# Optimization experiments

Measured on AMD Instinct MI355X. Metric: run time of the kernel, lower is better.

The kernel has to match this reference:

```python
import jax, jax.numpy as jnp
import numpy as np

B, C, E, HLR, WLR = 2, 64, 4, 192, 192


def setup_inputs() -> dict:
    key = jax.random.key(0)
    ks = jax.random.split(key, 8)
    s = 0.05  # keep activations/offsets in a sane range
    return {
        "x": jax.random.normal(ks[0], (B, C, HLR, WLR), jnp.float32),
        "fused": jax.random.normal(ks[1], (B, C, HLR, WLR), jnp.float32),
        "weight_compress": jax.random.normal(ks[2], (E, C // 8, C), jnp.float32) * s,
        "weight_expand": jax.random.normal(ks[3], (E, C, C // 8), jnp.float32) * s,
        "body_w1": jax.random.normal(ks[4], (64, 4), jnp.float32) * s,
        "body_b1": jnp.zeros((64,), jnp.float32),
        "body_w2": jax.random.normal(ks[5], (64, 64), jnp.float32) * s,
        "body_b2": jnp.zeros((64,), jnp.float32),
        "routing_w": jax.random.normal(ks[6], (E, 64), jnp.float32) * s,
        "routing_b": jnp.zeros((E,), jnp.float32),
        "offset_w": jax.random.normal(ks[7], (2, 64), jnp.float32) * s,
        "offset_b": jnp.zeros((2,), jnp.float32),
        "scale": 2,
    }


def _conv1x1(x, w, b):
    # x: [n, cin, H, W], w: [cout, cin] (1x1 conv)
    return jnp.einsum('oc,nchw->nohw', w, x) + b[None, :, None, None]


def _grid_sample(img, px, py):
    # Bilinear sample, align_corners=True semantics, zeros padding.
    # img: [b,c,h,w]; px, py: [b,H,W] absolute LR pixel coords.
    b, c, h, w = img.shape
    x0 = jnp.floor(px)
    y0 = jnp.floor(py)
    wx = (px - x0)[:, None]  # [b,1,H,W]
    wy = (py - y0)[:, None]

    def gather(xi, yi):
        valid = (xi >= 0) & (xi <= w - 1) & (yi >= 0) & (yi <= h - 1)
        xc = jnp.clip(xi, 0, w - 1).astype(jnp.int32)
        yc = jnp.clip(yi, 0, h - 1).astype(jnp.int32)
        v = jax.vmap(lambda im, yy, xx: im[:, yy, xx])(img, yc, xc)  # [b,c,H,W]
        return v * valid[:, None].astype(img.dtype)

    v00 = gather(x0, y0)
    v01 = gather(x0 + 1, y0)
    v10 = gather(x0, y0 + 1)
    v11 = gather(x0 + 1, y0 + 1)
    top = v00 * (1 - wx) + v01 * wx
    bot = v10 * (1 - wx) + v11 * wx
    return top * (1 - wy) + bot * wy


def reference(x, fused, weight_compress, weight_expand, body_w1, body_b1,
              body_w2, body_b2, routing_w, routing_b, offset_w, offset_b, scale):
    b, c, h, w = fused.shape
    H, W = round(h * scale), round(w * scale)
    e, c8 = weight_compress.shape[0], weight_compress.shape[1]

    ch = jnp.arange(H, dtype=jnp.float32)
    cw = jnp.arange(W, dtype=jnp.float32)
    coor_h = (ch + 0.5) / scale - jnp.floor((ch + 0.5) / scale + 0.001) - 0.5  # [H]
    coor_w = (cw + 0.5) / scale - jnp.floor((cw + 0.5) / scale + 0.001) - 0.5  # [W]
    inp = jnp.stack([
        jnp.full((H, W), 1.0 / scale, jnp.float32),
        jnp.full((H, W), 1.0 / scale, jnp.float32),
        jnp.broadcast_to(coor_h[:, None], (H, W)),
        jnp.broadcast_to(coor_w[None, :], (H, W)),
    ], 0)[None]  # [1,4,H,W]

    emb = jax.nn.relu(_conv1x1(inp, body_w1, body_b1))
    emb = jax.nn.relu(_conv1x1(emb, body_w2, body_b2))
    offset = _conv1x1(emb, offset_w, offset_b)            # [1,2,H,W]
    routing = jax.nn.sigmoid(_conv1x1(emb, routing_w, routing_b))  # [1,E,H,W]

    rw = routing.reshape(e, H * W).T                      # [HW, E]
    wc = (rw @ weight_compress.reshape(e, -1)).reshape(H, W, c8, c)  # per-pixel compress
    we = (rw @ weight_expand.reshape(e, -1)).reshape(H, W, c, c8)    # per-pixel expand

    # deformable sample: HR grid projected into LR space + learned offset (pixel units)
    px = jnp.broadcast_to((cw[None, :] + 0.5) / scale - 0.5, (H, W))[None] + offset[:, 0]
    py = jnp.broadcast_to((ch[:, None] + 0.5) / scale - 0.5, (H, W))[None] + offset[:, 1]
    px = jnp.broadcast_to(px, (b, H, W))
    py = jnp.broadcast_to(py, (b, H, W))
    fea0 = _grid_sample(fused, px, py)                    # [b,c,H,W]

    fea = fea0.transpose(0, 2, 3, 1)                      # [b,H,W,c]
    mid = jnp.einsum('hwoc,bhwc->bhwo', wc, fea)          # [b,H,W,c//8]
    out = jnp.einsum('hwco,bhwo->bhwc', we, mid)          # [b,H,W,c]
    return out.transpose(0, 3, 1, 2) + fea0
```

## Files before the change

### kernel.cpp

```cpp
#include <hip/hip_runtime.h>
#include <hip/hip_fp16.h>
#include <math.h>

typedef __attribute__((ext_vector_type(8))) _Float16 half8;
typedef __attribute__((ext_vector_type(4))) float f32x4;

#define HLR_ 192
#define WLR_ 192
#define H_ 384
#define W_ 384
#define LRP (HLR_*WLR_)
#define TPX 96
#define NTW (W_/TPX)
#define IPW 48
#define NCOL 52

#define WS_OFF_OFF 8192

__device__ __forceinline__ unsigned short f32_f16(float x){
    union { _Float16 h; unsigned short u; } c; c.h = (_Float16)x; return c.u;
}
__device__ __forceinline__ unsigned int pk_f16(float a, float b){
    union { _Float16 h[2]; unsigned int u; } c;
    c.h[0] = (_Float16)a; c.h[1] = (_Float16)b; return c.u;
}
__device__ __forceinline__ half8 splat8h(_Float16 h){
    half8 v = {h,h,h,h,h,h,h,h};
    return v;
}

__global__ __launch_bounds__(256) void prep_kernel(
    const float* __restrict__ w1, const float* __restrict__ b1,
    const float* __restrict__ w2, const float* __restrict__ b2,
    const float* __restrict__ rw, const float* __restrict__ rb,
    const float* __restrict__ ow, const float* __restrict__ ob,
    const float* __restrict__ WC, const float* __restrict__ WE,
    unsigned short* __restrict__ Kmat, float* __restrict__ g_off)
{
    __shared__ float smem[8912];
    int tid = threadIdx.x;

    float* sW2 = smem;
    float* sRW = smem + 4160;
    float* sE1 = smem + 4544;
    float* sR  = smem + 4800;
    float* sWc = smem + 4816;
    float* sWe = smem + 6864;

    for (int idx = tid; idx < 4096; idx += 256)
        sW2[(idx>>6)*65 + (idx&63)] = w2[idx];
    sRW[tid] = rw[tid];
    if (tid < 128) sRW[256 + tid] = ow[tid];

    int wave = tid >> 6, lane = tid & 63;
    int ph = wave >> 1, pw = wave & 1;

    float ch = (ph + 0.5f)*0.5f;
    float coor_h = ch - floorf(ch + 0.001f) - 0.5f;
    float cw = (pw + 0.5f)*0.5f;
    float coor_w = cw - floorf(cw + 0.001f) - 0.5f;

    float e1 = w1[lane*4+0]*0.5f + w1[lane*4+1]*0.5f
             + w1[lane*4+2]*coor_h + w1[lane*4+3]*coor_w + b1[lane];
    sE1[wave*64 + lane] = fmaxf(e1, 0.0f);
    __syncthreads();

    float e2 = b2[lane];
    #pragma unroll 16
    for (int i = 0; i < 64; ++i) e2 += sW2[lane*65 + i] * sE1[wave*64 + i];
    e2 = fmaxf(e2, 0.0f);

    #pragma unroll
    for (int k = 0; k < 6; ++k) {
        float t = sRW[k*64 + lane] * e2;
        #pragma unroll
        for (int m = 1; m <= 32; m <<= 1) t += __shfl_xor(t, m, 64);
        if (lane == 0) {
            if (k < 4) sR[wave*4 + k] = 1.0f/(1.0f + expf(-(t + rb[k])));
            else       g_off[wave*2 + (k-4)] = t + ob[k-4];
        }
    }
    __syncthreads();

    for (int idx = tid; idx < 2048; idx += 256) {
        int cls = idx >> 9, rem = idx & 511;
        float r0=sR[cls*4+0], r1=sR[cls*4+1], r2=sR[cls*4+2], r3=sR[cls*4+3];
        sWc[cls*512 + rem] =
            r0*WC[0*512+rem] + r1*WC[1*512+rem] + r2*WC[2*512+rem] + r3*WC[3*512+rem];
    }
    for (int idx = tid; idx < 2048; idx += 256) {
        int cls = idx >> 9, rem = idx & 511;
        float r0=sR[cls*4+0], r1=sR[cls*4+1], r2=sR[cls*4+2], r3=sR[cls*4+3];
        sWe[cls*512 + rem] =
            r0*WE[0*512+rem] + r1*WE[1*512+rem] + r2*WE[2*512+rem] + r3*WE[3*512+rem];
    }
    __syncthreads();

    for (int idx = tid; idx < 16384; idx += 256) {
        int cls = idx >> 12, rem = idx & 4095;
        int c = rem >> 6, cp = rem & 63;
        float a = (c == cp) ? 1.0f : 0.0f;
        #pragma unroll
        for (int o = 0; o < 8; ++o)
            a += sWe[cls*512 + c*8 + o] * sWc[cls*512 + o*64 + cp];
        Kmat[idx] = f32_f16(a);
    }
}

__global__ __launch_bounds__(256, 6) void main_kernel(
    const float* __restrict__ fused, const unsigned short* __restrict__ Kmat,
    const float* __restrict__ g_off, float* __restrict__ out)
{
    __shared__ unsigned short rowbuf[4*NCOL*64];

    int g = blockIdx.x;
    int xcd = g & 7;
    int t = g >> 3;
    int q = t >> 2;
    int wt = t & 3;
    int h = xcd*48 + q;
    int w0 = wt * TPX;
    int tid = threadIdx.x, wave = tid >> 6, lane = tid & 63;
    int b = wave >> 1, par = wave & 1;
    int ph = h & 1, cls = ph*2 + par;

    float off0 = g_off[cls*2 + 0];
    float off1 = g_off[cls*2 + 1];

    float py  = (h + 0.5f)*0.5f - 0.5f + off1;
    float y0f = floorf(py);
    float wy  = py - y0f;
    int   y0  = (int)y0f;
    float fy0 = (y0 >= 0  && y0 <= HLR_-1) ? 1.0f : 0.0f;
    float fy1 = (y0 >= -1 && y0 <= HLR_-2) ? 1.0f : 0.0f;
    int   yc0 = min(max(y0, 0), HLR_-1);
    int   yc1 = min(max(y0+1, 0), HLR_-1);
    float A0 = (1.0f - wy)*fy0;
    float A1 = wy*fy1;

    float pxb  = (w0 + par + 0.5f)*0.5f - 0.5f + off0;
    float x0bf = floorf(pxb);
    float wx   = pxb - x0bf;
    int   x0b  = (int)x0bf;
    float omwx = 1.0f - wx;

    int xbase = min(max(x0b, 0), WLR_-51);
    int dx = x0b - xbase;

    unsigned short* rw_base = rowbuf + wave*(NCOL*64);

    int cq  = lane >> 4;
    int xch = lane & 15;
    int x3  = xch & 3;
    if (xch < 13) {
        int xs_g = xbase + 4*xch;
        #pragma unroll 2
        for (int k = 0; k < 8; ++k) {
            int kk = (k + x3) & 7;
            int c0 = cq*16 + 2*kk;
            const float* p00 = fused + ((size_t)(b*64 + c0)*HLR_ + yc0)*WLR_ + xs_g;
            const float* p01 = fused + ((size_t)(b*64 + c0)*HLR_ + yc1)*WLR_ + xs_g;
            const float* p10 = p00 + LRP;
            const float* p11 = p01 + LRP;
            f32x4 a0, a1, b0, b1;
            if (xs_g <= WLR_-4) {
                a0 = *(const f32x4*)p00; a1 = *(const f32x4*)p01;
                b0 = *(const f32x4*)p10; b1 = *(const f32x4*)p11;
            } else {
                #pragma unroll
                for (int j = 0; j < 4; ++j) {
                    int xj = min(xs_g + j, WLR_-1) - xs_g;
                    a0[j] = p00[xj]; a1[j] = p01[xj];
                    b0[j] = p10[xj]; b1[j] = p11[xj];
                }
            }
            f32x4 e = a0*A0 + a1*A1;
            f32x4 f = b0*A0 + b1*A1;
            int chb = c0 >> 3, coff = c0 & 7;
            #pragma unroll
            for (int j = 0; j < 4; ++j) {
                int col = 4*xch + j;
                int chunk = chb ^ (col & 7);
                *(unsigned int*)(rw_base + col*64 + (chunk<<3) + coff) =
                    pk_f16(e[j], f[j]);
            }
        }
    }
    __syncthreads();

    int lm = lane & 15, lg = lane >> 4;

    const unsigned short* Kc = Kmat + cls*4096;
    half8 Af[4][2];
    #pragma unroll
    for (int mt = 0; mt < 4; ++mt)
        #pragma unroll
        for (int kt = 0; kt < 2; ++kt)
            Af[mt][kt] = *(const half8*)(Kc + (mt*16 + lm)*64 + kt*32 + lg*8);

    #pragma unroll
    for (int nt = 0; nt < 3; ++nt) {
        int slot = nt*16 + lm;
        int x_s = x0b + slot;
        float fxp = (x_s >= 0  && x_s <= WLR_-1) ? 1.0f : 0.0f;
        float fxn = (x_s >= -1 && x_s <= WLR_-2) ? 1.0f : 0.0f;
        int col  = min(max(slot + dx,     0), NCOL-1);
        int col1 = min(max(slot + 1 + dx, 0), NCOL-1);
        _Float16 W0 = (_Float16)(omwx * fxp);
        _Float16 W1 = (_Float16)(wx   * fxn);

        half8 P00 = *(const half8*)(rw_base + col *64 + (((0+lg) ^ (col &7))<<3));
        half8 P01 = *(const half8*)(rw_base + col1*64 + (((0+lg) ^ (col1&7))<<3));
        half8 P10 = *(const half8*)(rw_base + col *64 + (((4+lg) ^ (col &7))<<3));
        half8 P11 = *(const half8*)(rw_base + col1*64 + (((4+lg) ^ (col1&7))<<3));
        half8 B0 = P00*splat8h(W0) + P01*splat8h(W1);
        half8 B1 = P10*splat8h(W0) + P11*splat8h(W1);

        int wc = w0 + 2*slot + par;
        #pragma unroll
        for (int mt = 0; mt < 4; ++mt) {
            f32x4 a = {0.0f, 0.0f, 0.0f, 0.0f};
            a = __builtin_amdgcn_mfma_f32_16x16x32_f16(Af[mt][0], B0, a, 0, 0, 0);
            a = __builtin_amdgcn_mfma_f32_16x16x32_f16(Af[mt][1], B1, a, 0, 0, 0);
            int c0r = mt*16 + lg*4;
            float* op = out + (((size_t)(b*64 + c0r)*H_ + h)*W_ + wc);
            op[0*(size_t)(H_*W_)] = a[0];
            op[1*(size_t)(H_*W_)] = a[1];
            op[2*(size_t)(H_*W_)] = a[2];
            op[3*(size_t)(H_*W_)] = a[3];
        }
    }
}

extern "C" void kernel_launch(void* const* d_in, const int* in_sizes, int n_in,
                              void* d_out, int out_size, void* d_ws, size_t ws_size,
                              hipStream_t stream)
{
    const float* fused = (const float*)d_in[1];
    const float* WC    = (const float*)d_in[2];
    const float* WE    = (const float*)d_in[3];
    const float* w1    = (const float*)d_in[4];
    const float* b1    = (const float*)d_in[5];
    const float* w2    = (const float*)d_in[6];
    const float* b2    = (const float*)d_in[7];
    const float* rw    = (const float*)d_in[8];
    const float* rb    = (const float*)d_in[9];
    const float* ow    = (const float*)d_in[10];
    const float* ob    = (const float*)d_in[11];
    (void)in_sizes; (void)n_in; (void)out_size; (void)ws_size;

    float* ws = (float*)d_ws;
    unsigned short* Kmat = (unsigned short*)ws;
    float* g_off = ws + WS_OFF_OFF;
    float* o = (float*)d_out;

    hipLaunchKernelGGL(prep_kernel, dim3(1), dim3(256), 0, stream,
                       w1, b1, w2, b2, rw, rb, ow, ob, WC, WE, Kmat, g_off);
    hipLaunchKernelGGL(main_kernel, dim3(H_*NTW), dim3(256), 0, stream,
                       fused, Kmat, g_off, o);
}
```

Measured before the change: 164.9 us.

## Restructure LR row staging into wide batched vector loads per lane

Each lane now owns two channels and a 24-column span instead of looping over eight channel pairs. It issues all 28 float4 loads for both source rows up front, with the base aligned to a multiple of 4 so no bounds-checked scalar path is needed. The goal is more memory-level parallelism and fewer loop and branch overheads in the gather stage. In exchange it holds many more live registers, so the occupancy hint drops from 6 to 5 blocks. The 24-column span per half-wave may also create a less coalesced global access pattern.

```diff
diff --git a/kernel.cpp b/kernel.cpp
--- a/kernel.cpp
+++ b/kernel.cpp
@@ -14,6 +14,7 @@
 #define NTW (W_/TPX)
 #define IPW 48
 #define NCOL 52
+#define XBMAX (WLR_-NCOL)
 
 #define WS_OFF_OFF 8192
 
@@ -107,11 +108,11 @@
     }
 }
 
-__global__ __launch_bounds__(256, 6) void main_kernel(
+__global__ __launch_bounds__(256, 5) void main_kernel(
     const float* __restrict__ fused, const unsigned short* __restrict__ Kmat,
     const float* __restrict__ g_off, float* __restrict__ out)
 {
-    __shared__ unsigned short rowbuf[4*NCOL*64];
+    __shared__ __align__(16) unsigned short sFea[4*NCOL*64];
 
     int g = blockIdx.x;
     int xcd = g & 7;
@@ -144,46 +145,48 @@
     int   x0b  = (int)x0bf;
     float omwx = 1.0f - wx;
 
-    int xbase = min(max(x0b, 0), WLR_-51);
-    int dx = x0b - xbase;
-
-    unsigned short* rw_base = rowbuf + wave*(NCOL*64);
-
-    int cq  = lane >> 4;
-    int xch = lane & 15;
-    int x3  = xch & 3;
-    if (xch < 13) {
-        int xs_g = xbase + 4*xch;
-        #pragma unroll 2
-        for (int k = 0; k < 8; ++k) {
-            int kk = (k + x3) & 7;
-            int c0 = cq*16 + 2*kk;
-            const float* p00 = fused + ((size_t)(b*64 + c0)*HLR_ + yc0)*WLR_ + xs_g;
-            const float* p01 = fused + ((size_t)(b*64 + c0)*HLR_ + yc1)*WLR_ + xs_g;
-            const float* p10 = p00 + LRP;
-            const float* p11 = p01 + LRP;
-            f32x4 a0, a1, b0, b1;
-            if (xs_g <= WLR_-4) {
-                a0 = *(const f32x4*)p00; a1 = *(const f32x4*)p01;
-                b0 = *(const f32x4*)p10; b1 = *(const f32x4*)p11;
-            } else {
-                #pragma unroll
-                for (int j = 0; j < 4; ++j) {
-                    int xj = min(xs_g + j, WLR_-1) - xs_g;
-                    a0[j] = p00[xj]; a1[j] = p01[xj];
-                    b0[j] = p10[xj]; b1[j] = p11[xj];
-                }
-            }
-            f32x4 e = a0*A0 + a1*A1;
-            f32x4 f = b0*A0 + b1*A1;
-            int chb = c0 >> 3, coff = c0 & 7;
-            #pragma unroll
-            for (int j = 0; j < 4; ++j) {
-                int col = 4*xch + j;
-                int chunk = chb ^ (col & 7);
-                *(unsigned int*)(rw_base + col*64 + (chunk<<3) + coff) =
-                    pk_f16(e[j], f[j]);
-            }
+    int xbase4 = min(max(x0b, 0) & ~3, XBMAX);
+    int dx = x0b - xbase4;
+
+    unsigned short* rw_base = sFea + wave*(NCOL*64);
+
+    int xg   = lane >> 5;
+    int cp   = lane & 31;
+    int c0   = cp*2;
+    int colb = xg*24;
+
+    const float* base0 = fused + ((size_t)(b*64 + c0)*HLR_ + yc0)*WLR_ + xbase4 + colb;
+    const float* base1 = fused + ((size_t)(b*64 + c0)*HLR_ + yc1)*WLR_ + xbase4 + colb;
+
+    f32x4 e[7], f[7];
+    {
+        f32x4 r0v[7], r1v[7];
+        #pragma unroll
+        for (int v = 0; v < 7; ++v) r0v[v] = *(const f32x4*)(base0 + 4*v);
+        #pragma unroll
+        for (int v = 0; v < 7; ++v) r1v[v] = *(const f32x4*)(base1 + 4*v);
+        #pragma unroll
+        for (int v = 0; v < 7; ++v) e[v] = r0v[v]*A0 + r1v[v]*A1;
+    }
+    {
+        const float* q0p = base0 + LRP;
+        const float* q1p = base1 + LRP;
+        f32x4 r0v[7], r1v[7];
+        #pragma unroll
+        for (int v = 0; v < 7; ++v) r0v[v] = *(const f32x4*)(q0p + 4*v);
+        #pragma unroll
+        for (int v = 0; v < 7; ++v) r1v[v] = *(const f32x4*)(q1p + 4*v);
+        #pragma unroll
+        for (int v = 0; v < 7; ++v) f[v] = r0v[v]*A0 + r1v[v]*A1;
+    }
+    int chb = c0 >> 3, coff = c0 & 7;
+    #pragma unroll
+    for (int v = 0; v < 7; ++v) {
+        #pragma unroll
+        for (int j = 0; j < 4; ++j) {
+            int col = colb + 4*v + j;
+            *(unsigned int*)(rw_base + (col<<6) + ((chb ^ (col & 7))<<3) + coff) =
+                pk_f16(e[v][j], f[v][j]);
         }
     }
     __syncthreads();
@@ -209,10 +212,10 @@
         _Float16 W0 = (_Float16)(omwx * fxp);
         _Float16 W1 = (_Float16)(wx   * fxn);
 
-        half8 P00 = *(const half8*)(rw_base + col *64 + (((0+lg) ^ (col &7))<<3));
-        half8 P01 = *(const half8*)(rw_base + col1*64 + (((0+lg) ^ (col1&7))<<3));
-        half8 P10 = *(const half8*)(rw_base + col *64 + (((4+lg) ^ (col &7))<<3));
-        half8 P11 = *(const half8*)(rw_base + col1*64 + (((4+lg) ^ (col1&7))<<3));
+        half8 P00 = *(const half8*)(rw_base + (col <<6) + (((0+lg) ^ (col &7))<<3));
+        half8 P01 = *(const half8*)(rw_base + (col1<<6) + (((0+lg) ^ (col1&7))<<3));
+        half8 P10 = *(const half8*)(rw_base + (col <<6) + (((4+lg) ^ (col &7))<<3));
+        half8 P11 = *(const half8*)(rw_base + (col1<<6) + (((4+lg) ^ (col1&7))<<3));
         half8 B0 = P00*splat8h(W0) + P01*splat8h(W1);
         half8 B1 = P10*splat8h(W0) + P11*splat8h(W1);
 
```

New measurement: 160.4 us. 1.03x faster.
